# Performance work log

Hardware: AMD Instinct MI355X
Metric: run time of the kernel (lower is better)

## Reference

```python
import jax, jax.numpy as jnp
import numpy as np

N_NODES = 20000
N_EDGES = 320000
HEADS = 16
NEG_SLOPE = 0.2


def _gat_conv(x, src, dst, W, a_src, a_dst, b, heads, out_ch):
    # x: [N, F_in]; src/dst: [E'] (self-loops already appended)
    N = x.shape[0]
    h = (x @ W).reshape(N, heads, out_ch)                  # [N, H, C]
    alpha_s = jnp.sum(h * a_src, axis=-1)                  # [N, H]
    alpha_d = jnp.sum(h * a_dst, axis=-1)                  # [N, H]
    e = jax.nn.leaky_relu(alpha_s[src] + alpha_d[dst], NEG_SLOPE)  # [E', H]
    # segment softmax over edges grouped by destination node
    m = jax.ops.segment_max(e, dst, num_segments=N)        # [N, H]
    ex = jnp.exp(e - m[dst])
    denom = jax.ops.segment_sum(ex, dst, num_segments=N)
    alpha = ex / (denom[dst] + 1e-16)                      # [E', H]
    msg = h[src] * alpha[:, :, None]                       # [E', H, C]
    out = jax.ops.segment_sum(msg, dst, num_segments=N)    # [N, H, C]
    return out.reshape(N, heads * out_ch) + b


def _forward(x, edge_index, params):
    N = x.shape[0]
    loops = jnp.arange(N, dtype=edge_index.dtype)
    src = jnp.concatenate([edge_index[0], loops])
    dst = jnp.concatenate([edge_index[1], loops])
    for i, (W, a_s, a_d, b, out_ch) in enumerate(params):
        x = _gat_conv(x, src, dst, W, a_s, a_d, b, HEADS, out_ch)
        if i < len(params) - 1:
            x = jax.nn.relu(x)
    return jnp.sum(x, axis=0, keepdims=True)               # [1, 768]


def setup_inputs() -> dict:
    key = jax.random.key(0)
    ks = jax.random.split(key, 32)
    hid, heads, out_c = 64, HEADS, 3
    dims = [(3, hid), (hid * heads, hid), (hid * heads, hid), (hid * heads, hid), (hid * heads, hid), (hid * heads, out_c * heads)]
    inp = {}
    inp["x"] = jax.random.normal(ks[0], (N_NODES, 3), dtype=jnp.float32)
    inp["edge_index"] = jax.random.randint(ks[1], (2, N_EDGES), 0, N_NODES, dtype=jnp.int64)
    k = 2
    for li, (fin, c) in enumerate(dims, start=1):
        inp[f"W{li}"] = jax.random.normal(ks[k], (fin, heads * c), dtype=jnp.float32) * 0.1; k += 1
        inp[f"a{li}s"] = jax.random.normal(ks[k], (heads, c), dtype=jnp.float32) * 0.1; k += 1
        inp[f"a{li}d"] = jax.random.normal(ks[k], (heads, c), dtype=jnp.float32) * 0.1; k += 1
        inp[f"b{li}"] = jnp.zeros((heads * c,), dtype=jnp.float32)
    return inp


def reference(x, edge_index, W1, a1s, a1d, b1, W2, a2s, a2d, b2, W3, a3s, a3d, b3, W4, a4s, a4d, b4, W5, a5s, a5d, b5, W6, a6s, a6d, b6):
    params = [
        (W1, a1s, a1d, b1, 64), (W2, a2s, a2d, b2, 64), (W3, a3s, a3d, b3, 64),
        (W4, a4s, a4d, b4, 64), (W5, a5s, a5d, b5, 64), (W6, a6s, a6d, b6, 48),
    ]
    return _forward(x, edge_index, params)
```

## Files before the change

### kernel.cpp

```cpp
#include <hip/hip_runtime.h>
#include <cstddef>
#include <cstdint>

#define N_NODES 20000
#define N_EDGES 320000
#define E_TOT   (N_EDGES + N_NODES)
#define HEADS   16

typedef __bf16 bf16;
typedef __attribute__((ext_vector_type(8))) __bf16 bf16x8;
typedef __attribute__((ext_vector_type(4))) __bf16 bf16x4;
typedef __attribute__((ext_vector_type(4))) float  f32x4;

__device__ __forceinline__ void gll16(const void* g, void* l) {
    __builtin_amdgcn_global_load_lds(
        (const __attribute__((address_space(1))) unsigned int*)g,
        (__attribute__((address_space(3))) unsigned int*)l, 16, 0, 0);
}

__global__ __launch_bounds__(256)
void k_lin1(const float* __restrict__ x, const float* __restrict__ W,
            const float* __restrict__ aS, const float* __restrict__ aD,
            bf16* __restrict__ hg, float* __restrict__ as_,
            float* __restrict__ ad_) {
    int n = blockIdx.x;
    int t = threadIdx.x;
    int f0 = t * 4, hd = t >> 4;
    float x0 = x[n*3+0], x1 = x[n*3+1], x2 = x[n*3+2];
    float v[4];
    bf16x4 hv;
#pragma unroll
    for (int c = 0; c < 4; ++c) {
        int f = f0 + c;
        v[c] = x0*W[f] + x1*W[1024+f] + x2*W[2048+f];
        hv[c] = (bf16)v[c];
    }
    *reinterpret_cast<bf16x4*>(&hg[(size_t)n * 1024 + f0]) = hv;
    float ps = 0.f, pd = 0.f;
    int cb = (t & 15) * 4;
#pragma unroll
    for (int c = 0; c < 4; ++c) {
        ps = fmaf(v[c], aS[hd*64 + cb + c], ps);
        pd = fmaf(v[c], aD[hd*64 + cb + c], pd);
    }
#pragma unroll
    for (int off = 1; off < 16; off <<= 1) {
        ps += __shfl_xor(ps, off);
        pd += __shfl_xor(pd, off);
    }
    if ((t & 15) == 0) {
        as_[n*16 + hd] = ps;
        ad_[n*16 + hd] = pd;
    }
}

__global__ __launch_bounds__(256)
void k_convW(const float* __restrict__ W, bf16* __restrict__ Th,
             bf16* __restrict__ Tl, int M) {
    __shared__ float t[32][33];
    int m0 = blockIdx.x * 32, k0 = blockIdx.y * 32;
    int j = threadIdx.x & 31, i0 = threadIdx.x >> 5;
#pragma unroll
    for (int s = 0; s < 4; ++s) {
        int i = i0 + s * 8;
        t[i][j] = W[(size_t)(k0 + i) * M + m0 + j];
    }
    __syncthreads();
#pragma unroll
    for (int s = 0; s < 4; ++s) {
        int i = i0 + s * 8;
        float v = t[j][i];
        bf16 hi = (bf16)v;
        Th[(size_t)(m0 + i) * 1024 + k0 + j] = hi;
        if (Tl) Tl[(size_t)(m0 + i) * 1024 + k0 + j] = (bf16)(v - (float)hi);
    }
}

template<bool FUSE, bool TWOB>
__global__ __launch_bounds__(256, 2)
void k_gemm3(const bf16* __restrict__ Ah,
             const bf16* __restrict__ Bh, const bf16* __restrict__ Bl,
             float* __restrict__ Cf, bf16* __restrict__ Ch,
             const float* __restrict__ aS, const float* __restrict__ aD,
             float* __restrict__ as_, float* __restrict__ ad_,
             int N, int M) {
    __shared__ __align__(16) bf16 sAh[128 * 32];
    __shared__ __align__(16) bf16 sBh[128 * 32];
    __shared__ __align__(16) bf16 sBl[TWOB ? 128 * 32 : 8];

    const int tid  = threadIdx.x;
    const int wid  = tid >> 6, lane = tid & 63;
    const int wr   = wid >> 1, wc = wid & 1;
    const int col0 = blockIdx.x * 128, row0 = blockIdx.y * 128;

    f32x4 acc[4][4] = {};

    const int rl = lane >> 2;
    const int gg = lane & 3;
    const int rb0 = wid * 32;
    const int lrow = lane & 15, g4 = lane >> 4;

    for (int k0 = 0; k0 < 1024; k0 += 32) {
#pragma unroll
        for (int half = 0; half < 2; ++half) {
            int rt = rb0 + half * 16 + rl;
            int kc = (gg ^ ((rt >> 1) & 3)) * 8;
            size_t lbase = (size_t)(rb0 + half * 16) * 32;
            int ar = row0 + rt; if (ar >= N) ar = N - 1;
            gll16(Ah + (size_t)ar * 1024 + k0 + kc, sAh + lbase);
            int br = col0 + rt;
            gll16(Bh + (size_t)br * 1024 + k0 + kc, sBh + lbase);
            if (TWOB) gll16(Bl + (size_t)br * 1024 + k0 + kc, sBl + lbase);
        }
        __syncthreads();

        bf16x8 ah[4], bh[4], bl[4];
#pragma unroll
        for (int m = 0; m < 4; ++m) {
            int r = wr * 64 + m * 16 + lrow;
            int off = r * 32 + ((g4 ^ ((r >> 1) & 3)) * 8);
            ah[m] = *(const bf16x8*)&sAh[off];
        }
#pragma unroll
        for (int n = 0; n < 4; ++n) {
            int r = wc * 64 + n * 16 + lrow;
            int off = r * 32 + ((g4 ^ ((r >> 1) & 3)) * 8);
            bh[n] = *(const bf16x8*)&sBh[off];
            if (TWOB) bl[n] = *(const bf16x8*)&sBl[off];
        }
#pragma unroll
        for (int m = 0; m < 4; ++m)
#pragma unroll
            for (int n = 0; n < 4; ++n) {
                acc[m][n] = __builtin_amdgcn_mfma_f32_16x16x32_bf16(ah[m], bh[n], acc[m][n], 0, 0, 0);
                if (TWOB)
                    acc[m][n] = __builtin_amdgcn_mfma_f32_16x16x32_bf16(ah[m], bl[n], acc[m][n], 0, 0, 0);
            }
        __syncthreads();
    }

#pragma unroll
    for (int m = 0; m < 4; ++m) {
#pragma unroll
        for (int n = 0; n < 4; ++n) {
            int col = col0 + wc * 64 + n * 16 + lrow;
#pragma unroll
            for (int q = 0; q < 4; ++q) {
                int row = row0 + wr * 64 + m * 16 + g4 * 4 + q;
                if (row < N) {
                    float v = acc[m][n][q];
                    if (!FUSE) Cf[(size_t)row * M + col] = v;
                    Ch[(size_t)row * M + col] = (bf16)v;
                }
            }
        }
    }

    if (FUSE) {
        const int hd = blockIdx.x * 2 + wc;
        float asv[4], adv[4];
#pragma unroll
        for (int n = 0; n < 4; ++n) {
            asv[n] = aS[hd * 64 + n * 16 + lrow];
            adv[n] = aD[hd * 64 + n * 16 + lrow];
        }
        float ps[4][4], pd[4][4];
#pragma unroll
        for (int m = 0; m < 4; ++m)
#pragma unroll
            for (int q = 0; q < 4; ++q) {
                float s = 0.f, d = 0.f;
#pragma unroll
                for (int n = 0; n < 4; ++n) {
                    s = fmaf(acc[m][n][q], asv[n], s);
                    d = fmaf(acc[m][n][q], adv[n], d);
                }
                ps[m][q] = s; pd[m][q] = d;
            }
#pragma unroll
        for (int off = 1; off < 16; off <<= 1) {
#pragma unroll
            for (int m = 0; m < 4; ++m)
#pragma unroll
                for (int q = 0; q < 4; ++q) {
                    ps[m][q] += __shfl_xor(ps[m][q], off);
                    pd[m][q] += __shfl_xor(pd[m][q], off);
                }
        }
        if (lrow == 0) {
#pragma unroll
            for (int m = 0; m < 4; ++m)
#pragma unroll
                for (int q = 0; q < 4; ++q) {
                    int row = row0 + wr * 64 + m * 16 + g4 * 4 + q;
                    if (row < N) {
                        as_[row * 16 + hd] = ps[m][q];
                        ad_[row * 16 + hd] = pd[m][q];
                    }
                }
        }
    }
}

__global__ __launch_bounds__(256)
void k_alpha(const float* __restrict__ h, const float* __restrict__ a_s,
             const float* __restrict__ a_d, float* __restrict__ as_out,
             float* __restrict__ ad_out, int C, int M) {
    int pair = blockIdx.x * 4 + (threadIdx.x >> 6);
    int lane = threadIdx.x & 63;
    if (pair >= N_NODES * HEADS) return;
    int n = pair >> 4, hd = pair & 15;
    float vs = 0.f, vd = 0.f;
    if (lane < C) {
        float hv = h[(size_t)n * M + hd * C + lane];
        vs = hv * a_s[hd * C + lane];
        vd = hv * a_d[hd * C + lane];
    }
#pragma unroll
    for (int off = 32; off > 0; off >>= 1) {
        vs += __shfl_down(vs, off);
        vd += __shfl_down(vd, off);
    }
    if (lane == 0) { as_out[pair] = vs; ad_out[pair] = vd; }
}

__global__ void k_zero_i(int* __restrict__ p, int n) {
    int t = blockIdx.x * 256 + threadIdx.x;
    if (t < n) p[t] = 0;
}
__global__ void k_hist(const int* __restrict__ ei, int* __restrict__ deg) {
    int e = blockIdx.x * 256 + threadIdx.x;
    if (e >= E_TOT) return;
    int d = (e < N_EDGES) ? ei[N_EDGES + e] : e - N_EDGES;
    atomicAdd(&deg[d], 1);
}
__global__ __launch_bounds__(256)
void k_scan(const int* __restrict__ deg, int* __restrict__ rowstart,
            int* __restrict__ cursor) {
    __shared__ int sh[256];
    int carry = 0;
    for (int base = 0; base < N_NODES; base += 256) {
        int i = base + threadIdx.x;
        int v = (i < N_NODES) ? deg[i] : 0;
        sh[threadIdx.x] = v;
        __syncthreads();
        for (int off = 1; off < 256; off <<= 1) {
            int t = (threadIdx.x >= off) ? sh[threadIdx.x - off] : 0;
            __syncthreads();
            sh[threadIdx.x] += t;
            __syncthreads();
        }
        if (i < N_NODES) {
            int excl = carry + sh[threadIdx.x] - v;
            rowstart[i] = excl;
            cursor[i] = excl;
        }
        carry += sh[255];
        __syncthreads();
    }
    if (threadIdx.x == 0) rowstart[N_NODES] = carry;
}
__global__ void k_scatter(const int* __restrict__ ei, int* __restrict__ cursor,
                          int* __restrict__ csr_src) {
    int e = blockIdx.x * 256 + threadIdx.x;
    if (e >= E_TOT) return;
    int s, d;
    if (e < N_EDGES) { s = ei[e]; d = ei[N_EDGES + e]; }
    else             { s = d = e - N_EDGES; }
    int slot = atomicAdd(&cursor[d], 1);
    csr_src[slot] = s;
}

__global__ __launch_bounds__(256)
void k_alpha_edge(const int* __restrict__ rowstart, const int* __restrict__ csr_src,
                  const float* __restrict__ as_, const float* __restrict__ ad_,
                  float* __restrict__ alpha) {
    int t = blockIdx.x * 256 + threadIdx.x;
    if (t >= N_NODES * HEADS) return;
    int n = t >> 4, hd = t & 15;
    int s0 = rowstart[n], s1 = rowstart[n + 1];
    float adv = ad_[t];
    float m = -1e30f, den = 0.f;
    for (int j = s0; j < s1; ++j) {
        float v = as_[csr_src[j] * 16 + hd] + adv;
        v = v > 0.f ? v : 0.2f * v;
        float nm = fmaxf(m, v);
        float rm = __expf(m - nm);
        float re = __expf(v - nm);
        den = den * rm + re;
        m = nm;
    }
    float inv = 1.f / (den + 1e-16f);
    for (int j = s0; j < s1; ++j) {
        float v = as_[csr_src[j] * 16 + hd] + adv;
        v = v > 0.f ? v : 0.2f * v;
        alpha[(size_t)j * 16 + hd] = __expf(v - m) * inv;
    }
}

__global__ __launch_bounds__(256)
void k_agg1024(const bf16* __restrict__ hg, const int* __restrict__ rowstart,
               const int* __restrict__ csr_src, const float* __restrict__ alpha,
               const float* __restrict__ bias, bf16* __restrict__ oh) {
    int n = blockIdx.y * 16 + (threadIdx.x >> 4);
    int sub = threadIdx.x & 15;
    int f0 = blockIdx.x * 128 + sub * 8;
    int hd = f0 >> 6;
    int s0 = rowstart[n], s1 = rowstart[n + 1];
    float acc[8] = {};
#pragma unroll 2
    for (int j = s0; j < s1; ++j) {
        int s = csr_src[j];
        float a = alpha[(size_t)j * 16 + hd];
        bf16x8 hv = *reinterpret_cast<const bf16x8*>(&hg[(size_t)s * 1024 + f0]);
#pragma unroll
        for (int c = 0; c < 8; ++c)
            acc[c] = fmaf(a, (float)hv[c], acc[c]);
    }
    bf16x8 vh;
#pragma unroll
    for (int c = 0; c < 8; ++c) {
        float r = fmaxf(acc[c] + bias[f0 + c], 0.f);
        vh[c] = (bf16)r;
    }
    *reinterpret_cast<bf16x8*>(&oh[(size_t)n * 1024 + f0]) = vh;
}

__global__ __launch_bounds__(256)
void k_agg768(const bf16* __restrict__ hg, const int* __restrict__ rowstart,
              const int* __restrict__ csr_src, const float* __restrict__ alpha,
              const float* __restrict__ bias, float* __restrict__ out) {
    int n = blockIdx.x * 2 + (threadIdx.x >> 7);
    int tloc = threadIdx.x & 127;
    if (tloc >= 96) return;
    int f0 = tloc * 8;
    int hd = f0 / 48;
    int s0 = rowstart[n], s1 = rowstart[n + 1];
    float acc[8] = {};
#pragma unroll 2
    for (int j = s0; j < s1; ++j) {
        int s = csr_src[j];
        float a = alpha[(size_t)j * 16 + hd];
        bf16x8 hv = *reinterpret_cast<const bf16x8*>(&hg[(size_t)s * 768 + f0]);
#pragma unroll
        for (int c = 0; c < 8; ++c)
            acc[c] = fmaf(a, (float)hv[c], acc[c]);
    }
#pragma unroll
    for (int c = 0; c < 8; ++c)
        out[(size_t)n * 768 + f0 + c] = acc[c] + bias[f0 + c];
}

__global__ __launch_bounds__(256)
void k_colsum(const float* __restrict__ x, float* __restrict__ out) {
    int f = blockIdx.x * 256 + threadIdx.x;
    int chunk = blockIdx.y;
    int n0 = chunk * 625, n1 = n0 + 625;
    float s = 0.f;
    for (int n = n0; n < n1; ++n) s += x[(size_t)n * 768 + f];
    atomicAdd(&out[f], s);
}

extern "C" void kernel_launch(void* const* d_in, const int* in_sizes, int n_in,
                              void* d_out, int out_size, void* d_ws, size_t ws_size,
                              hipStream_t stream) {
    const float* x0 = (const float*)d_in[0];
    const int*   ei = (const int*)d_in[1];

    char* w = (char*)d_ws;
    float* xB  = (float*)w;
    float* xOut = (float*)w;
    w += (size_t)N_NODES * 1024 * sizeof(float);
    bf16*  hgat = (bf16*)w; w += (size_t)N_NODES * 1024 * sizeof(bf16);
    bf16*  x_hi = (bf16*)w; w += (size_t)N_NODES * 1024 * sizeof(bf16);
    float* as_  = (float*)w; w += (size_t)N_NODES * HEADS * sizeof(float);
    float* ad_  = (float*)w; w += (size_t)N_NODES * HEADS * sizeof(float);
    float* alpha = (float*)w; w += (size_t)E_TOT * HEADS * sizeof(float);
    bf16* Wt_hi = (bf16*)w; w += (size_t)1024 * 1024 * sizeof(bf16);
    bf16* Wt_lo = (bf16*)w; w += (size_t)1024 * 1024 * sizeof(bf16);
    int* deg      = (int*)w; w += N_NODES * sizeof(int);
    int* rowstart = (int*)w; w += (N_NODES + 1) * sizeof(int);
    int* cursor   = (int*)w; w += N_NODES * sizeof(int);
    int* csr_src  = (int*)w; w += E_TOT * sizeof(int);

    k_zero_i<<<(N_NODES + 255) / 256, 256, 0, stream>>>(deg, N_NODES);
    k_hist<<<(E_TOT + 255) / 256, 256, 0, stream>>>(ei, deg);
    k_scan<<<1, 256, 0, stream>>>(deg, rowstart, cursor);
    k_scatter<<<(E_TOT + 255) / 256, 256, 0, stream>>>(ei, cursor, csr_src);

    for (int l = 0; l < 6; ++l) {
        const float* W  = (const float*)d_in[2 + 4 * l + 0];
        const float* aS = (const float*)d_in[2 + 4 * l + 1];
        const float* aD = (const float*)d_in[2 + 4 * l + 2];
        const float* bv = (const float*)d_in[2 + 4 * l + 3];
        int M = (l == 5) ? 768 : 1024;

        if (l == 0) {
            k_lin1<<<N_NODES, 256, 0, stream>>>(x0, W, aS, aD, hgat, as_, ad_);
        } else {
            dim3 tg(M / 32, 32);
            dim3 grid(M / 128, (N_NODES + 127) / 128);
            if (l < 5) {
                k_convW<<<tg, 256, 0, stream>>>(W, Wt_hi, nullptr, M);
                k_gemm3<true, false><<<grid, 256, 0, stream>>>(
                    x_hi, Wt_hi, nullptr, nullptr, hgat, aS, aD, as_, ad_,
                    N_NODES, M);
            } else {
                k_convW<<<tg, 256, 0, stream>>>(W, Wt_hi, Wt_lo, M);
                k_gemm3<false, true><<<grid, 256, 0, stream>>>(
                    x_hi, Wt_hi, Wt_lo, xB, hgat, nullptr, nullptr,
                    nullptr, nullptr, N_NODES, M);
                k_alpha<<<(N_NODES * HEADS + 3) / 4, 256, 0, stream>>>(
                    xB, aS, aD, as_, ad_, 48, 768);
            }
        }
        k_alpha_edge<<<(N_NODES * HEADS + 255) / 256, 256, 0, stream>>>(
            rowstart, csr_src, as_, ad_, alpha);
        if (l < 5) {
            dim3 agrid(8, N_NODES / 16);
            k_agg1024<<<agrid, 256, 0, stream>>>(
                hgat, rowstart, csr_src, alpha, bv, x_hi);
        } else {
            k_agg768<<<N_NODES / 2, 256, 0, stream>>>(
                hgat, rowstart, csr_src, alpha, bv, xOut);
        }
    }

    hipMemsetAsync(d_out, 0, (size_t)out_size * sizeof(float), stream);
    dim3 cgrid(3, 32);
    k_colsum<<<cgrid, 256, 0, stream>>>(xOut, (float*)d_out);
}
```

Before: 1.297 ms.

## Split edge softmax into parallel max/denominator and per-edge alpha kernels; stage GEMM stores

```diff
diff --git a/kernel.cpp b/kernel.cpp
--- a/kernel.cpp
+++ b/kernel.cpp
@@ -139,18 +139,20 @@
         __syncthreads();
     }
 
-#pragma unroll
-    for (int m = 0; m < 4; ++m) {
-#pragma unroll
-        for (int n = 0; n < 4; ++n) {
-            int col = col0 + wc * 64 + n * 16 + lrow;
-#pragma unroll
-            for (int q = 0; q < 4; ++q) {
-                int row = row0 + wr * 64 + m * 16 + g4 * 4 + q;
-                if (row < N) {
-                    float v = acc[m][n][q];
-                    if (!FUSE) Cf[(size_t)row * M + col] = v;
-                    Ch[(size_t)row * M + col] = (bf16)v;
+    if (!FUSE) {
+#pragma unroll
+        for (int m = 0; m < 4; ++m) {
+#pragma unroll
+            for (int n = 0; n < 4; ++n) {
+                int col = col0 + wc * 64 + n * 16 + lrow;
+#pragma unroll
+                for (int q = 0; q < 4; ++q) {
+                    int row = row0 + wr * 64 + m * 16 + g4 * 4 + q;
+                    if (row < N) {
+                        float v = acc[m][n][q];
+                        Cf[(size_t)row * M + col] = v;
+                        Ch[(size_t)row * M + col] = (bf16)v;
+                    }
                 }
             }
         }
@@ -198,6 +200,32 @@
                         ad_[row * 16 + hd] = pd[m][q];
                     }
                 }
+        }
+
+        bf16* sC = sAh;
+#pragma unroll
+        for (int m = 0; m < 4; ++m) {
+            __syncthreads();
+#pragma unroll
+            for (int n = 0; n < 4; ++n) {
+#pragma unroll
+                for (int q = 0; q < 4; ++q) {
+                    int rh = wr * 16 + g4 * 4 + q;
+                    int cc = wc * 64 + n * 16 + lrow;
+                    sC[rh * 128 + cc] = (bf16)acc[m][n][q];
+                }
+            }
+            __syncthreads();
+#pragma unroll
+            for (int it = 0; it < 2; ++it) {
+                int rh = it * 16 + (tid >> 4);
+                int cc = (tid & 15) * 8;
+                int grow = row0 + (rh >> 4) * 64 + m * 16 + (rh & 15);
+                if (grow < N) {
+                    bf16x8 vv = *reinterpret_cast<const bf16x8*>(&sC[rh * 128 + cc]);
+                    *reinterpret_cast<bf16x8*>(&Ch[(size_t)grow * M + col0 + cc]) = vv;
+                }
+            }
         }
     }
 }
@@ -261,7 +289,7 @@
     if (threadIdx.x == 0) rowstart[N_NODES] = carry;
 }
 __global__ void k_scatter(const int* __restrict__ ei, int* __restrict__ cursor,
-                          int* __restrict__ csr_src) {
+                          int* __restrict__ csr_src, int* __restrict__ csr_dst) {
     int e = blockIdx.x * 256 + threadIdx.x;
     if (e >= E_TOT) return;
     int s, d;
@@ -269,19 +297,21 @@
     else             { s = d = e - N_EDGES; }
     int slot = atomicAdd(&cursor[d], 1);
     csr_src[slot] = s;
-}
-
-__global__ __launch_bounds__(256)
-void k_alpha_edge(const int* __restrict__ rowstart, const int* __restrict__ csr_src,
-                  const float* __restrict__ as_, const float* __restrict__ ad_,
-                  float* __restrict__ alpha) {
-    int t = blockIdx.x * 256 + threadIdx.x;
-    if (t >= N_NODES * HEADS) return;
-    int n = t >> 4, hd = t & 15;
+    csr_dst[slot] = d;
+}
+
+__global__ __launch_bounds__(256)
+void k_mden(const int* __restrict__ rowstart, const int* __restrict__ csr_src,
+            const float* __restrict__ as_, const float* __restrict__ ad_,
+            float* __restrict__ m_, float* __restrict__ inv_) {
+    int n = blockIdx.x * 4 + (threadIdx.x >> 6);
+    int lane = threadIdx.x & 63;
+    int hd = lane & 15;
+    int strip = lane >> 4;
     int s0 = rowstart[n], s1 = rowstart[n + 1];
-    float adv = ad_[t];
+    float adv = ad_[n * 16 + hd];
     float m = -1e30f, den = 0.f;
-    for (int j = s0; j < s1; ++j) {
+    for (int j = s0 + strip; j < s1; j += 4) {
         float v = as_[csr_src[j] * 16 + hd] + adv;
         v = v > 0.f ? v : 0.2f * v;
         float nm = fmaxf(m, v);
@@ -290,12 +320,32 @@
         den = den * rm + re;
         m = nm;
     }
-    float inv = 1.f / (den + 1e-16f);
-    for (int j = s0; j < s1; ++j) {
-        float v = as_[csr_src[j] * 16 + hd] + adv;
-        v = v > 0.f ? v : 0.2f * v;
-        alpha[(size_t)j * 16 + hd] = __expf(v - m) * inv;
-    }
+#pragma unroll
+    for (int off = 16; off <= 32; off <<= 1) {
+        float mo = __shfl_xor(m, off);
+        float dn = __shfl_xor(den, off);
+        float nm = fmaxf(m, mo);
+        den = den * __expf(m - nm) + dn * __expf(mo - nm);
+        m = nm;
+    }
+    if (strip == 0) {
+        m_[n * 16 + hd] = m;
+        inv_[n * 16 + hd] = 1.f / (den + 1e-16f);
+    }
+}
+
+__global__ __launch_bounds__(256)
+void k_alpha_w(const int* __restrict__ csr_src, const int* __restrict__ csr_dst,
+               const float* __restrict__ as_, const float* __restrict__ ad_,
+               const float* __restrict__ m_, const float* __restrict__ inv_,
+               float* __restrict__ alpha) {
+    int t = blockIdx.x * 256 + threadIdx.x;
+    if (t >= E_TOT * HEADS) return;
+    int j = t >> 4, hd = t & 15;
+    int s = csr_src[j], d = csr_dst[j];
+    float v = as_[s * 16 + hd] + ad_[d * 16 + hd];
+    v = v > 0.f ? v : 0.2f * v;
+    alpha[t] = __expf(v - m_[d * 16 + hd]) * inv_[d * 16 + hd];
 }
 
 __global__ __launch_bounds__(256)
@@ -375,6 +425,8 @@
     bf16*  x_hi = (bf16*)w; w += (size_t)N_NODES * 1024 * sizeof(bf16);
     float* as_  = (float*)w; w += (size_t)N_NODES * HEADS * sizeof(float);
     float* ad_  = (float*)w; w += (size_t)N_NODES * HEADS * sizeof(float);
+    float* m_   = (float*)w; w += (size_t)N_NODES * HEADS * sizeof(float);
+    float* inv_ = (float*)w; w += (size_t)N_NODES * HEADS * sizeof(float);
     float* alpha = (float*)w; w += (size_t)E_TOT * HEADS * sizeof(float);
     bf16* Wt_hi = (bf16*)w; w += (size_t)1024 * 1024 * sizeof(bf16);
     bf16* Wt_lo = (bf16*)w; w += (size_t)1024 * 1024 * sizeof(bf16);
@@ -382,11 +434,12 @@
     int* rowstart = (int*)w; w += (N_NODES + 1) * sizeof(int);
     int* cursor   = (int*)w; w += N_NODES * sizeof(int);
     int* csr_src  = (int*)w; w += E_TOT * sizeof(int);
+    int* csr_dst  = (int*)w; w += E_TOT * sizeof(int);
 
     k_zero_i<<<(N_NODES + 255) / 256, 256, 0, stream>>>(deg, N_NODES);
     k_hist<<<(E_TOT + 255) / 256, 256, 0, stream>>>(ei, deg);
     k_scan<<<1, 256, 0, stream>>>(deg, rowstart, cursor);
-    k_scatter<<<(E_TOT + 255) / 256, 256, 0, stream>>>(ei, cursor, csr_src);
+    k_scatter<<<(E_TOT + 255) / 256, 256, 0, stream>>>(ei, cursor, csr_src, csr_dst);
 
     for (int l = 0; l < 6; ++l) {
         const float* W  = (const float*)d_in[2 + 4 * l + 0];
@@ -414,8 +467,9 @@
                     xB, aS, aD, as_, ad_, 48, 768);
             }
         }
-        k_alpha_edge<<<(N_NODES * HEADS + 255) / 256, 256, 0, stream>>>(
-            rowstart, csr_src, as_, ad_, alpha);
+        k_mden<<<N_NODES / 4, 256, 0, stream>>>(rowstart, csr_src, as_, ad_, m_, inv_);
+        k_alpha_w<<<(E_TOT * HEADS + 255) / 256, 256, 0, stream>>>(
+            csr_src, csr_dst, as_, ad_, m_, inv_, alpha);
         if (l < 5) {
             dim3 agrid(8, N_NODES / 16);
             k_agg1024<<<agrid, 256, 0, stream>>>(
```

Result: no change. 1.285 ms (-0.9%).
